# Kernel tuning notes

Measured on AMD Instinct MI355X. Metric: run time of the kernel, lower is better.

## Reference

```python
import jax, jax.numpy as jnp
import numpy as np

B, S, D, H = 2, 2048, 128, 8  # batch, seq, num_hidden(=head dim), num_heads
EPS = 1e-5


def setup_inputs() -> dict:
    key = jax.random.key(0)
    ks = jax.random.split(key, 12)
    sc = 0.02
    return {
        "query": jax.random.normal(ks[0], (B, S, D), dtype=jnp.float32),
        "Wq": jax.random.normal(ks[1], (2 * H * D, D), dtype=jnp.float32) * sc,
        "bq": jnp.zeros((2 * H * D,), dtype=jnp.float32),
        "Wk": jax.random.normal(ks[2], (2 * H * D, D), dtype=jnp.float32) * sc,
        "bk": jnp.zeros((2 * H * D,), dtype=jnp.float32),
        "Wv": jax.random.normal(ks[3], (H * D, D), dtype=jnp.float32) * sc,
        "bv": jnp.zeros((H * D,), dtype=jnp.float32),
        "Wo": jax.random.normal(ks[4], (D, H * D), dtype=jnp.float32) * sc,
        "bo": jnp.zeros((D,), dtype=jnp.float32),
        "gn_w": jnp.ones((H,), dtype=jnp.float32),
        "gn_b": jnp.zeros((H,), dtype=jnp.float32),
        "lam": jax.random.uniform(ks[5], (), dtype=jnp.float32),
    }


def reference(query, Wq, bq, Wk, bk, Wv, bv, Wo, bo, gn_w, gn_b, lam):
    # Faithful to the torch module: the .view calls are raw reshapes (no
    # transpose), d_k=1 so scale is 1, mask=None path (no causal mask),
    # dropout in eval mode, _lambda == _lambda_init == lam.
    q = (query @ Wq.T + bq).reshape(B, H, S, 2 * D)
    k = (query @ Wk.T + bk).reshape(B, H, S, 2 * D)
    v = (query @ Wv.T + bv).reshape(B, H, S, D)
    q1, q2 = q[..., :D], q[..., D:]
    k1, k2 = k[..., :D], k[..., D:]
    s1 = jnp.einsum("bhqd,bhkd->bhqk", q1, k1)  # / sqrt(d_k=1)
    s2 = jnp.einsum("bhqd,bhkd->bhqk", q2, k2)
    attn = jax.nn.softmax(s1, axis=-1) - lam * jax.nn.softmax(s2, axis=-1)
    out = jnp.einsum("bhqk,bhkd->bhqd", attn, v)          # (B,H,S,D)
    out = out.transpose(0, 2, 1, 3).reshape(B, H, S, D)   # faithful raw reshape
    # GroupNorm(num_groups=H, num_channels=H): normalize per (b, h) over (S, D)
    mean = out.mean(axis=(2, 3), keepdims=True)
    var = out.var(axis=(2, 3), keepdims=True)
    out = (out - mean) * jax.lax.rsqrt(var + EPS)
    out = out * gn_w[None, :, None, None] + gn_b[None, :, None, None]
    out = out * (1.0 - lam)
    # torch.cat([out[:, i] for i in range(H)], dim=-1) -> (B, S, H*D)
    out = out.transpose(0, 2, 1, 3).reshape(B, S, H * D)
    return out @ Wo.T + bo
```

## Files before the change

### kernel.cpp

```cpp
#include <hip/hip_runtime.h>

typedef __bf16 bf16x8 __attribute__((ext_vector_type(8)));
typedef __bf16 bf16x4 __attribute__((ext_vector_type(4)));
typedef float  f32x4  __attribute__((ext_vector_type(4)));

#define MFMA16(a,b,c) __builtin_amdgcn_mfma_f32_16x16x32_bf16((a),(b),(c),0,0,0)

__device__ __forceinline__ bf16x8 cvt8(float4 a, float4 b) {
  bf16x8 v;
  v[0]=(__bf16)a.x; v[1]=(__bf16)a.y; v[2]=(__bf16)a.z; v[3]=(__bf16)a.w;
  v[4]=(__bf16)b.x; v[5]=(__bf16)b.y; v[6]=(__bf16)b.z; v[7]=(__bf16)b.w;
  return v;
}
__device__ __forceinline__ bf16x4 cvt4(float4 a) {
  bf16x4 v;
  v[0]=(__bf16)a.x; v[1]=(__bf16)a.y; v[2]=(__bf16)a.z; v[3]=(__bf16)a.w;
  return v;
}


__global__ void to_bf16(const float* __restrict__ q,  const float* __restrict__ wq,
                        const float* __restrict__ wk, const float* __restrict__ wv,
                        __bf16* __restrict__ qb,  __bf16* __restrict__ wqb,
                        __bf16* __restrict__ wkb, __bf16* __restrict__ wvb)
{
  const long e = (long)(blockIdx.x * 256 + threadIdx.x) * 8;
  const float* src; __bf16* dst; long off;
  if (e < 524288)       { src = q;  dst = qb;  off = e; }
  else if (e < 786432)  { src = wq; dst = wqb; off = e - 524288; }
  else if (e < 1048576) { src = wk; dst = wkb; off = e - 786432; }
  else                  { src = wv; dst = wvb; off = e - 1048576; }
  *(bf16x8*)(dst + off) = cvt8(*(const float4*)(src + off), *(const float4*)(src + off + 4));
}

#define LDA 136
__global__ __launch_bounds__(256, 2) void qkv_gemm(
    const __bf16* __restrict__ queryb,
    const __bf16* __restrict__ Wqb, const float* __restrict__ bq,
    const __bf16* __restrict__ Wkb, const float* __restrict__ bk,
    const __bf16* __restrict__ Wvb, const float* __restrict__ bv,
    __bf16* __restrict__ Qbf, __bf16* __restrict__ Kbf, __bf16* __restrict__ Vbf)
{
  __shared__ __bf16 As[128 * LDA];
  __shared__ __bf16 Bs[128 * LDA];
  const int t = threadIdx.x;
  const int tile = blockIdx.x;
  const int tm = tile / 40, tn = tile % 40;
  const int m0 = tm * 128, n0 = tn * 128;

  const __bf16* wbase; const float* bias;
  __bf16* obase; int ocol0; int ostride; float oscale;
  if (n0 < 2048)      { wbase = Wqb + n0*128;        bias = bq + n0;        obase = Qbf; ocol0 = n0;      ostride = 2048; oscale = 1.4426950408889634f; }
  else if (n0 < 4096) { wbase = Wkb + (n0-2048)*128; bias = bk + (n0-2048); obase = Kbf; ocol0 = n0-2048; ostride = 2048; oscale = 1.0f; }
  else                { wbase = Wvb + (n0-4096)*128; bias = bv + (n0-4096); obase = Vbf; ocol0 = n0-4096; ostride = 1024; oscale = 1.0f; }

  const __bf16* abase = queryb + (long)m0 * 128;
  for (int r = 0; r < 2; ++r) {
    int e = (r*256 + t) * 32;
    int row = e >> 7, col = e & 127;
    #pragma unroll
    for (int c = 0; c < 4; ++c) {
      *(bf16x8*)&As[row*LDA + col + c*8] = *(const bf16x8*)(abase + (long)row*128 + col + c*8);
      *(bf16x8*)&Bs[row*LDA + col + c*8] = *(const bf16x8*)(wbase + (long)row*128 + col + c*8);
    }
  }
  __syncthreads();

  const int w = t >> 6, lane = t & 63;
  const int lo = lane & 15, quad = lane >> 4;
  const int wm = w >> 1, wn = w & 1;

  f32x4 acc[4][4];
  #pragma unroll
  for (int i = 0; i < 4; ++i)
    #pragma unroll
    for (int j = 0; j < 4; ++j) acc[i][j] = (f32x4){0.f,0.f,0.f,0.f};

  #pragma unroll
  for (int ks = 0; ks < 4; ++ks) {
    bf16x8 af[4], bfr[4];
    #pragma unroll
    for (int i = 0; i < 4; ++i)
      af[i] = *(const bf16x8*)&As[(wm*64 + i*16 + lo)*LDA + ks*32 + quad*8];
    #pragma unroll
    for (int j = 0; j < 4; ++j)
      bfr[j] = *(const bf16x8*)&Bs[(wn*64 + j*16 + lo)*LDA + ks*32 + quad*8];
    #pragma unroll
    for (int i = 0; i < 4; ++i)
      #pragma unroll
      for (int j = 0; j < 4; ++j)
        acc[i][j] = MFMA16(bfr[j], af[i], acc[i][j]);
  }
  #pragma unroll
  for (int j = 0; j < 4; ++j) {
    const int colb = ocol0 + wn*64 + j*16 + quad*4;
    const f32x4 b4 = *(const f32x4*)(bias + wn*64 + j*16 + quad*4);
    #pragma unroll
    for (int i = 0; i < 4; ++i) {
      const int row = m0 + wm*64 + i*16 + lo;
      bf16x4 v;
      #pragma unroll
      for (int r = 0; r < 4; ++r) v[r] = (__bf16)((acc[i][j][r] + b4[r]) * oscale);
      *(bf16x4*)&obase[(long)row*ostride + colb] = v;
    }
  }
}

__global__ void v_transpose(const __bf16* __restrict__ Vbf, __bf16* __restrict__ Vt)
{
  __shared__ __bf16 tile[128 * 136];
  const int t = threadIdx.x;
  const int bh = blockIdx.x >> 4, st = blockIdx.x & 15;
  const __bf16* src = Vbf + (long)bh*262144 + st*16384;
  for (int r = 0; r < 8; ++r) {
    int e = (r*256 + t) * 8;
    int row = e >> 7, col = e & 127;
    *(bf16x8*)&tile[row*136 + col] = *(const bf16x8*)(src + row*128 + col);
  }
  __syncthreads();
  __bf16* dst = Vt + (long)bh*262144 + st*128;
  for (int r = 0; r < 8; ++r) {
    int e = (r*256 + t) * 8;
    int d = e >> 7, s2c = e & 127;
    bf16x8 v;
    #pragma unroll
    for (int i = 0; i < 8; ++i) v[i] = tile[(s2c + i)*136 + d];
    *(bf16x8*)(dst + d*2048 + s2c) = v;
  }
}

#define LDK 264
#define LDV 40
__global__ __launch_bounds__(256, 2) void attn(
    const __bf16* __restrict__ Qbf, const __bf16* __restrict__ Kbf,
    const __bf16* __restrict__ Vt, float* __restrict__ O,
    const float* __restrict__ lam_p, float* __restrict__ stats)
{
  __shared__ __bf16 Ks[2][32 * LDK];
  __shared__ __bf16 Vs[2][128 * LDV];
  __shared__ float red[8];
  const int t = threadIdx.x;
  const int w = t >> 6, lane = t & 63;
  const int lo = lane & 15, quad = lane >> 4;
  const int bh = blockIdx.x & 15, qb = blockIdx.x >> 4;
  const float lam = *lam_p;

  const __bf16* Qh = Qbf + (long)bh*524288;
  const __bf16* Kh = Kbf + (long)bh*524288;
  const __bf16* Vh = Vt  + (long)bh*262144;
  const int qrow0 = qb*64 + w*16;

  bf16x8 qf[8];
  #pragma unroll
  for (int ks = 0; ks < 8; ++ks)
    qf[ks] = *(const bf16x8*)(Qh + (long)(qrow0 + lo)*256 + ks*32 + quad*8);

  int ke[2], ksrow[2], kcol[2], vdd[2], vch[2];
  #pragma unroll
  for (int r = 0; r < 2; ++r) {
    ke[r] = (r*256 + t) * 16;
    const int row = ke[r] >> 8;
    kcol[r] = ke[r] & 255;
    ksrow[r] = (row & 3) + ((row >> 2) & 1)*16 + ((row >> 3) & 3)*4;
    const int c = r*256 + t;
    vdd[r] = c >> 2; vch[r] = c & 3;
  }

  bf16x8 kra[2][2], vra[2];
  #pragma unroll
  for (int r = 0; r < 2; ++r) {
    kra[r][0] = *(const bf16x8*)(Kh + ke[r]);
    kra[r][1] = *(const bf16x8*)(Kh + ke[r] + 8);
    vra[r]    = *(const bf16x8*)(Vh + (long)vdd[r]*2048 + vch[r]*8);
  }
  #pragma unroll
  for (int r = 0; r < 2; ++r) {
    *(bf16x8*)&Ks[0][ksrow[r]*LDK + kcol[r]]     = kra[r][0];
    *(bf16x8*)&Ks[0][ksrow[r]*LDK + kcol[r] + 8] = kra[r][1];
    *(bf16x8*)&Vs[0][vdd[r]*LDV + vch[r]*8]      = vra[r];
  }

  f32x4 acc[2][8];
  #pragma unroll
  for (int s = 0; s < 2; ++s)
    #pragma unroll
    for (int mt = 0; mt < 8; ++mt) acc[s][mt] = (f32x4){0.f,0.f,0.f,0.f};
  float lsum[2] = {0.f, 0.f};

  for (int kt = 0; kt < 64; ++kt) {
    __syncthreads();
    if (kt + 1 < 64) {
      #pragma unroll
      for (int r = 0; r < 2; ++r) {
        kra[r][0] = *(const bf16x8*)(Kh + (long)(kt+1)*8192 + ke[r]);
        kra[r][1] = *(const bf16x8*)(Kh + (long)(kt+1)*8192 + ke[r] + 8);
        vra[r]    = *(const bf16x8*)(Vh + (long)vdd[r]*2048 + (kt+1)*32 + vch[r]*8);
      }
    }
    const __bf16* kb = Ks[kt & 1];
    const __bf16* vb = Vs[kt & 1];

    f32x4 s1[2], s2[2];
    #pragma unroll
    for (int nt = 0; nt < 2; ++nt) { s1[nt] = (f32x4){0.f,0.f,0.f,0.f}; s2[nt] = (f32x4){0.f,0.f,0.f,0.f}; }
    #pragma unroll
    for (int nt = 0; nt < 2; ++nt) {
      const int krow = lo + nt*16;
      #pragma unroll
      for (int ks = 0; ks < 4; ++ks) {
        bf16x8 kf = *(const bf16x8*)&kb[krow*LDK + ks*32 + quad*8];
        s1[nt] = MFMA16(kf, qf[ks], s1[nt]);
      }
      #pragma unroll
      for (int ks = 4; ks < 8; ++ks) {
        bf16x8 kf = *(const bf16x8*)&kb[krow*LDK + ks*32 + quad*8];
        s2[nt] = MFMA16(kf, qf[ks], s2[nt]);
      }
    }

    bf16x8 pf1, pf2;
    #pragma unroll
    for (int nt = 0; nt < 2; ++nt) {
      #pragma unroll
      for (int r = 0; r < 4; ++r) {
        float p0 = __builtin_exp2f(s1[nt][r]);
        float p1 = __builtin_exp2f(s2[nt][r]);
        lsum[0] += p0;
        lsum[1] += p1;
        pf1[nt*4+r] = (__bf16)p0;
        pf2[nt*4+r] = (__bf16)p1;
      }
    }

    #pragma unroll
    for (int mt = 0; mt < 8; ++mt) {
      bf16x8 vf = *(const bf16x8*)&vb[(mt*16 + lo)*LDV + quad*8];
      acc[0][mt] = MFMA16(vf, pf1, acc[0][mt]);
      acc[1][mt] = MFMA16(vf, pf2, acc[1][mt]);
    }

    if (kt + 1 < 64) {
      __bf16* kn = Ks[(kt+1) & 1];
      __bf16* vn = Vs[(kt+1) & 1];
      #pragma unroll
      for (int r = 0; r < 2; ++r) {
        *(bf16x8*)&kn[ksrow[r]*LDK + kcol[r]]     = kra[r][0];
        *(bf16x8*)&kn[ksrow[r]*LDK + kcol[r] + 8] = kra[r][1];
        *(bf16x8*)&vn[vdd[r]*LDV + vch[r]*8]      = vra[r];
      }
    }
  }

  #pragma unroll
  for (int s = 0; s < 2; ++s) {
    lsum[s] += __shfl_xor(lsum[s], 16);
    lsum[s] += __shfl_xor(lsum[s], 32);
  }
  const float inv1 = 1.f / lsum[0];
  const float inv2 = lam / lsum[1];

  float ssum = 0.f, ssq = 0.f;
  float* Oh = O + (long)bh*262144;
  #pragma unroll
  for (int mt = 0; mt < 8; ++mt) {
    f32x4 o;
    #pragma unroll
    for (int r = 0; r < 4; ++r) {
      o[r] = acc[0][mt][r]*inv1 - acc[1][mt][r]*inv2;
      ssum += o[r]; ssq += o[r]*o[r];
    }
    *(f32x4*)(Oh + (long)(qrow0 + lo)*128 + mt*16 + quad*4) = o;
  }
  #pragma unroll
  for (int msk = 1; msk < 64; msk <<= 1) { ssum += __shfl_xor(ssum, msk); ssq += __shfl_xor(ssq, msk); }
  if (lane == 0) { red[w] = ssum; red[4 + w] = ssq; }
  __syncthreads();
  if (t == 0) {
    const int g = (bh >> 3)*8 + (qb >> 2);
    atomicAdd(&stats[g*2],   red[0] + red[1] + red[2] + red[3]);
    atomicAdd(&stats[g*2+1], red[4] + red[5] + red[6] + red[7]);
  }
}

#define LDC 72
__global__ __launch_bounds__(256, 2) void out_gemm(
    const float* __restrict__ O, const float* __restrict__ stats,
    const float* __restrict__ gn_w, const float* __restrict__ gn_b,
    const float* __restrict__ lam_p,
    const float* __restrict__ Wo, const float* __restrict__ bo,
    float* __restrict__ out)
{
  __shared__ __bf16 As[64 * LDC];
  __shared__ __bf16 Bs[128 * LDC];
  const int t = threadIdx.x;
  const int w = t >> 6, lane = t & 63;
  const int lo = lane & 15, quad = lane >> 4;
  const int m0 = (blockIdx.x & 63) * 64;
  const int kq = blockIdx.x >> 6;
  const int b = m0 >> 11;
  const float lam1 = 1.f - *lam_p;

  const int hp = kq;
  const float sN   = stats[(b*8 + hp)*2];
  const float ssN  = stats[(b*8 + hp)*2 + 1];
  const float mean = sN * (1.f/262144.f);
  const float rstd = rsqrtf(ssN * (1.f/262144.f) - mean*mean + 1e-5f);
  const float gwv  = gn_w[hp] * rstd * lam1;
  const float shv  = (gn_b[hp] - mean * rstd * gn_w[hp]) * lam1;

  f32x4 acc[8];
  #pragma unroll
  for (int j = 0; j < 8; ++j) acc[j] = (f32x4){0.f,0.f,0.f,0.f};

  for (int kc = 0; kc < 2; ++kc) {
    const int k0 = kq*128 + kc*64;
    const int d0 = kc*64;
    __syncthreads();
    for (int r = 0; r < 4; ++r) {
      int e = r*1024 + t*4;
      int row_l = e >> 6, col_l = e & 63;
      const int spp = (m0 + row_l) & 2047;
      const int h = spp & 7, srow = hp*256 + (spp >> 3);
      float4 v = *(const float4*)(O + ((long)(b*8 + h)*2048 + srow)*128 + d0 + col_l);
      float4 o;
      o.x = v.x*gwv + shv; o.y = v.y*gwv + shv; o.z = v.z*gwv + shv; o.w = v.w*gwv + shv;
      *(bf16x4*)&As[row_l*LDC + col_l] = cvt4(o);
    }
    for (int r = 0; r < 8; ++r) {
      int e = (r*256 + t) * 4;
      int row = e >> 6, col = e & 63;
      *(bf16x4*)&Bs[row*LDC + col] = cvt4(*(const float4*)(Wo + (long)row*1024 + k0 + col));
    }
    __syncthreads();
    #pragma unroll
    for (int ks = 0; ks < 2; ++ks) {
      bf16x8 af = *(const bf16x8*)&As[(w*16 + lo)*LDC + ks*32 + quad*8];
      #pragma unroll
      for (int j = 0; j < 8; ++j) {
        bf16x8 bfr = *(const bf16x8*)&Bs[(j*16 + lo)*LDC + ks*32 + quad*8];
        acc[j] = MFMA16(af, bfr, acc[j]);
      }
    }
  }
  #pragma unroll
  for (int j = 0; j < 8; ++j) {
    const int col = j*16 + lo;
    const float bb = bo[col] * 0.125f;
    #pragma unroll
    for (int r = 0; r < 4; ++r)
      atomicAdd(&out[(long)(m0 + w*16 + quad*4 + r)*128 + col], acc[j][r] + bb);
  }
}

extern "C" void kernel_launch(void* const* d_in, const int* in_sizes, int n_in,
                              void* d_out, int out_size, void* d_ws, size_t ws_size,
                              hipStream_t stream) {
  const float* query = (const float*)d_in[0];
  const float* Wq = (const float*)d_in[1];
  const float* bq = (const float*)d_in[2];
  const float* Wk = (const float*)d_in[3];
  const float* bk = (const float*)d_in[4];
  const float* Wv = (const float*)d_in[5];
  const float* bv = (const float*)d_in[6];
  const float* Wo = (const float*)d_in[7];
  const float* bo = (const float*)d_in[8];
  const float* gn_w = (const float*)d_in[9];
  const float* gn_b = (const float*)d_in[10];
  const float* lam = (const float*)d_in[11];

  char* ws = (char*)d_ws;
  __bf16* Qbf   = (__bf16*)(ws);
  __bf16* Kbf   = (__bf16*)(ws + (16l<<20));
  __bf16* Vbf   = (__bf16*)(ws + (32l<<20));
  __bf16* Vt    = (__bf16*)(ws + (40l<<20));
  float*  O     = (float* )(ws + (48l<<20));
  __bf16* queryb= (__bf16*)(ws + (64l<<20));
  __bf16* Wqb   = (__bf16*)(ws + (65l<<20));
  __bf16* Wkb   = (__bf16*)(ws + (65l<<20) + (512l<<10));
  __bf16* Wvb   = (__bf16*)(ws + (66l<<20));
  float*  stats = (float* )(ws + (66l<<20) + (256l<<10));
  float* out = (float*)d_out;

  to_bf16    <<<dim3(576),  dim3(256), 0, stream>>>(query, Wq, Wk, Wv, queryb, Wqb, Wkb, Wvb);
  qkv_gemm   <<<dim3(1280), dim3(256), 0, stream>>>(queryb, Wqb, bq, Wkb, bk, Wvb, bv, Qbf, Kbf, Vbf);
  v_transpose<<<dim3(256),  dim3(256), 0, stream>>>(Vbf, Vt);
  attn       <<<dim3(512),  dim3(256), 0, stream>>>(Qbf, Kbf, Vt, O, lam, stats);
  out_gemm   <<<dim3(512),  dim3(256), 0, stream>>>(O, stats, gn_w, gn_b, lam, Wo, bo, out);
}
```

Baseline: 216.5 us.

## Split attention waves by softmax branch and share K fragments across two query tiles

Each wave now handles one of the two differential-attention branches (q1/k1 or q2/k2) for 32 query rows, instead of both branches for 16 rows. Each K fragment read from shared memory now feeds two MFMAs, which halves K LDS traffic per MFMA and cuts the per-wave Q fragment registers from eight to eight-in-two-tiles of four. The two branches are combined at the end through a shared-memory exchange, which adds extra syncs and an LDS round trip in the epilogue. The V fragment reuse stays the same.

```diff
diff --git a/kernel.cpp b/kernel.cpp
--- a/kernel.cpp
+++ b/kernel.cpp
@@ -142,18 +142,21 @@
   const int t = threadIdx.x;
   const int w = t >> 6, lane = t & 63;
   const int lo = lane & 15, quad = lane >> 4;
+  const int s = w & 1, qg = w >> 1;
   const int bh = blockIdx.x & 15, qb = blockIdx.x >> 4;
   const float lam = *lam_p;
 
   const __bf16* Qh = Qbf + (long)bh*524288;
   const __bf16* Kh = Kbf + (long)bh*524288;
   const __bf16* Vh = Vt  + (long)bh*262144;
-  const int qrow0 = qb*64 + w*16;
-
-  bf16x8 qf[8];
-  #pragma unroll
-  for (int ks = 0; ks < 8; ++ks)
-    qf[ks] = *(const bf16x8*)(Qh + (long)(qrow0 + lo)*256 + ks*32 + quad*8);
+  const int qrow0 = qb*64 + qg*32;
+
+  bf16x8 qf[2][4];
+  #pragma unroll
+  for (int qt = 0; qt < 2; ++qt)
+    #pragma unroll
+    for (int ks = 0; ks < 4; ++ks)
+      qf[qt][ks] = *(const bf16x8*)(Qh + (long)(qrow0 + qt*16 + lo)*256 + s*128 + ks*32 + quad*8);
 
   int ke[2], ksrow[2], kcol[2], vdd[2], vch[2];
   #pragma unroll
@@ -182,9 +185,9 @@
 
   f32x4 acc[2][8];
   #pragma unroll
-  for (int s = 0; s < 2; ++s)
-    #pragma unroll
-    for (int mt = 0; mt < 8; ++mt) acc[s][mt] = (f32x4){0.f,0.f,0.f,0.f};
+  for (int qt = 0; qt < 2; ++qt)
+    #pragma unroll
+    for (int mt = 0; mt < 8; ++mt) acc[qt][mt] = (f32x4){0.f,0.f,0.f,0.f};
   float lsum[2] = {0.f, 0.f};
 
   for (int kt = 0; kt < 64; ++kt) {
@@ -200,43 +203,41 @@
     const __bf16* kb = Ks[kt & 1];
     const __bf16* vb = Vs[kt & 1];
 
-    f32x4 s1[2], s2[2];
-    #pragma unroll
-    for (int nt = 0; nt < 2; ++nt) { s1[nt] = (f32x4){0.f,0.f,0.f,0.f}; s2[nt] = (f32x4){0.f,0.f,0.f,0.f}; }
+    f32x4 sf[2][2];
+    #pragma unroll
+    for (int qt = 0; qt < 2; ++qt)
+      #pragma unroll
+      for (int nt = 0; nt < 2; ++nt) sf[qt][nt] = (f32x4){0.f,0.f,0.f,0.f};
     #pragma unroll
     for (int nt = 0; nt < 2; ++nt) {
       const int krow = lo + nt*16;
       #pragma unroll
       for (int ks = 0; ks < 4; ++ks) {
-        bf16x8 kf = *(const bf16x8*)&kb[krow*LDK + ks*32 + quad*8];
-        s1[nt] = MFMA16(kf, qf[ks], s1[nt]);
-      }
-      #pragma unroll
-      for (int ks = 4; ks < 8; ++ks) {
-        bf16x8 kf = *(const bf16x8*)&kb[krow*LDK + ks*32 + quad*8];
-        s2[nt] = MFMA16(kf, qf[ks], s2[nt]);
-      }
-    }
-
-    bf16x8 pf1, pf2;
-    #pragma unroll
-    for (int nt = 0; nt < 2; ++nt) {
-      #pragma unroll
-      for (int r = 0; r < 4; ++r) {
-        float p0 = __builtin_exp2f(s1[nt][r]);
-        float p1 = __builtin_exp2f(s2[nt][r]);
-        lsum[0] += p0;
-        lsum[1] += p1;
-        pf1[nt*4+r] = (__bf16)p0;
-        pf2[nt*4+r] = (__bf16)p1;
+        bf16x8 kf = *(const bf16x8*)&kb[krow*LDK + s*128 + ks*32 + quad*8];
+        sf[0][nt] = MFMA16(kf, qf[0][ks], sf[0][nt]);
+        sf[1][nt] = MFMA16(kf, qf[1][ks], sf[1][nt]);
+      }
+    }
+
+    bf16x8 pf[2];
+    #pragma unroll
+    for (int qt = 0; qt < 2; ++qt) {
+      #pragma unroll
+      for (int nt = 0; nt < 2; ++nt) {
+        #pragma unroll
+        for (int r = 0; r < 4; ++r) {
+          float p = __builtin_exp2f(sf[qt][nt][r]);
+          lsum[qt] += p;
+          pf[qt][nt*4+r] = (__bf16)p;
+        }
       }
     }
 
     #pragma unroll
     for (int mt = 0; mt < 8; ++mt) {
       bf16x8 vf = *(const bf16x8*)&vb[(mt*16 + lo)*LDV + quad*8];
-      acc[0][mt] = MFMA16(vf, pf1, acc[0][mt]);
-      acc[1][mt] = MFMA16(vf, pf2, acc[1][mt]);
+      acc[0][mt] = MFMA16(vf, pf[0], acc[0][mt]);
+      acc[1][mt] = MFMA16(vf, pf[1], acc[1][mt]);
     }
 
     if (kt + 1 < 64) {
@@ -252,24 +253,46 @@
   }
 
   #pragma unroll
-  for (int s = 0; s < 2; ++s) {
-    lsum[s] += __shfl_xor(lsum[s], 16);
-    lsum[s] += __shfl_xor(lsum[s], 32);
-  }
-  const float inv1 = 1.f / lsum[0];
-  const float inv2 = lam / lsum[1];
+  for (int qt = 0; qt < 2; ++qt) {
+    lsum[qt] += __shfl_xor(lsum[qt], 16);
+    lsum[qt] += __shfl_xor(lsum[qt], 32);
+  }
+  float inv[2];
+  const float nume = (s == 0) ? 1.f : lam;
+  inv[0] = nume / lsum[0];
+  inv[1] = nume / lsum[1];
+
+  float* fs = (float*)Ks;
+  __syncthreads();
+  if (s == 1) {
+    #pragma unroll
+    for (int qt = 0; qt < 2; ++qt)
+      #pragma unroll
+      for (int mt = 0; mt < 8; ++mt) {
+        f32x4 o;
+        #pragma unroll
+        for (int r = 0; r < 4; ++r) o[r] = acc[qt][mt][r] * inv[qt];
+        *(f32x4*)&fs[(qg*32 + qt*16 + lo)*132 + mt*16 + quad*4] = o;
+      }
+  }
+  __syncthreads();
 
   float ssum = 0.f, ssq = 0.f;
-  float* Oh = O + (long)bh*262144;
-  #pragma unroll
-  for (int mt = 0; mt < 8; ++mt) {
-    f32x4 o;
-    #pragma unroll
-    for (int r = 0; r < 4; ++r) {
-      o[r] = acc[0][mt][r]*inv1 - acc[1][mt][r]*inv2;
-      ssum += o[r]; ssq += o[r]*o[r];
-    }
-    *(f32x4*)(Oh + (long)(qrow0 + lo)*128 + mt*16 + quad*4) = o;
+  if (s == 0) {
+    float* Oh = O + (long)bh*262144;
+    #pragma unroll
+    for (int qt = 0; qt < 2; ++qt)
+      #pragma unroll
+      for (int mt = 0; mt < 8; ++mt) {
+        f32x4 o2 = *(const f32x4*)&fs[(qg*32 + qt*16 + lo)*132 + mt*16 + quad*4];
+        f32x4 o;
+        #pragma unroll
+        for (int r = 0; r < 4; ++r) {
+          o[r] = acc[qt][mt][r]*inv[qt] - o2[r];
+          ssum += o[r]; ssq += o[r]*o[r];
+        }
+        *(f32x4*)(Oh + (long)(qrow0 + qt*16 + lo)*128 + mt*16 + quad*4) = o;
+      }
   }
   #pragma unroll
   for (int msk = 1; msk < 64; msk <<= 1) { ssum += __shfl_xor(ssum, msk); ssq += __shfl_xor(ssq, msk); }
```

New measurement: 206.6 us. -4.6%, faster.
